# Optimization experiments

Measured on AMD Instinct MI355X. Metric: run time of the kernel, lower is better.

## Reference

```python
import jax, jax.numpy as jnp
import numpy as np

EPS = 1e-10

def _pairwise_cos_dist(X, Y):
    # X: (N, c), Y: (M, c) -> (N, M) cosine distance, matching torch impl exactly
    x_norm = jnp.sqrt(jnp.sum(X * X, axis=1, keepdims=True))          # (N, 1)
    y_norm = jnp.sqrt(jnp.sum(Y * Y, axis=1, keepdims=True)).T        # (1, M)
    return 1.0 - (X @ Y.T) / (x_norm + EPS) / (y_norm + EPS)

def _style_loss_cos(X, Y):
    D = _pairwise_cos_dist(X, Y)
    m1 = jnp.min(D, axis=1).mean()  # relaxed EMD, row mins
    m2 = jnp.min(D, axis=0).mean()  # col mins
    return jnp.maximum(m1, m2)

def _moment_loss(X, Y):
    # X, Y: (N, c)
    n = X.shape[0]
    mu_x = X.mean(axis=0, keepdims=True)
    mu_y = Y.mean(axis=0, keepdims=True)
    mu_d = jnp.abs(mu_x - mu_y).mean()
    Xc = X - mu_x
    Yc = Y - mu_y
    X_cov = (Xc.T @ Xc) / (n - 1)   # (c, c)
    Y_cov = (Yc.T @ Yc) / (n - 1)
    return mu_d + jnp.abs(X_cov - Y_cov).mean()

def _level_loss(X, Y):
    # X, Y: (N, c) per-batch, per-level feature sets
    return _style_loss_cos(X, Y) + _moment_loss(X, Y)

_per_batch_level_loss = jax.vmap(_level_loss)  # over leading batch dim

def _gather_points(feat, idx):
    # feat: (B, c, h, w), idx: (B, N) spatial indices -> (B, N, c)
    B, c, h, w = feat.shape
    flat = feat.reshape(B, c, h * w)
    g = jnp.take_along_axis(flat, idx[:, None, :], axis=2)  # (B, c, N)
    return jnp.swapaxes(g, 1, 2)

def _all_points(feat):
    # feat: (B, c, h, w) -> (B, h*w, c); used when h <= 32 (no subsampling)
    B, c, h, w = feat.shape
    return jnp.swapaxes(feat.reshape(B, c, h * w), 1, 2)

def setup_inputs() -> dict:
    key = jax.random.key(0)
    ks = jax.random.split(key, 11)
    shapes = [(8, 64, 256, 256), (8, 128, 128, 128), (8, 256, 64, 64), (8, 512, 32, 32)]
    inp = {}
    for i, s in enumerate(shapes):
        inp[f"target_feat{i}"] = jax.random.normal(ks[i], s, dtype=jnp.float32)
        inp[f"gen_feat{i}"] = jax.random.normal(ks[4 + i], s, dtype=jnp.float32)
    for j, hw in enumerate([256 * 256, 128 * 128, 64 * 64]):
        inp[f"idx{j}"] = jnp.sort(
            jax.random.randint(ks[8 + j], (8, 1000), 0, hw, dtype=jnp.int32), axis=1
        )
    return inp

def reference(target_feat0, target_feat1, target_feat2, target_feat3,
              gen_feat0, gen_feat1, gen_feat2, gen_feat3,
              idx0, idx1, idx2):
    B = target_feat0.shape[0]
    loss_b = jnp.zeros((B,), dtype=target_feat0.dtype)
    # levels 0-2: h > 32 -> subsample 1000 spatial points
    for t, g, idx in [(target_feat0, gen_feat0, idx0),
                      (target_feat1, gen_feat1, idx1),
                      (target_feat2, gen_feat2, idx2)]:
        loss_b = loss_b + _per_batch_level_loss(_gather_points(t, idx), _gather_points(g, idx))
    # level 3: h == 32 -> use all 1024 points
    loss_b = loss_b + _per_batch_level_loss(_all_points(target_feat3), _all_points(gen_feat3))
    return loss_b.mean()  # sum over batch / batch_size
```

## Files before the change

### kernel.cpp

```cpp
#include <hip/hip_runtime.h>
#include <cstdint>
#include <cstddef>

#define EPSC 1e-10f
typedef unsigned short u16;
typedef unsigned int u32;
typedef __attribute__((ext_vector_type(8))) short bf16x8;
typedef __attribute__((ext_vector_type(4))) float f32x4;

#define XTX_B 0u
#define XTY_B 7864320u
#define XNX_B 15728640u
#define XNY_B 23592960u
#define FB 15728640u
#define RNX_OFF (FB + 0u)
#define RNY_OFF (FB + 32768u)
#define RMIN_OFF (FB + 65536u)
#define CMIN_OFF (FB + 98304u)
#define MUX_OFF (FB + 131072u)
#define MUY_OFF (FB + 138752u)
#define COVS_OFF (FB + 146432u)
#define ACC_OFF (FB + 146464u)

struct Tabs { int c[4], N[4], mo[4]; u32 off[4]; };
struct GArgs {
  const float* t[4];
  const float* g[4];
  const int* idx[4];
  int c[4], hw[4], N[4];
  u32 off[4];
};

__device__ __forceinline__ u16 f2bf(float f) {
  u32 u = __float_as_uint(f);
  u = (u + 0x7fffu + ((u >> 16) & 1u)) >> 16;
  return (u16)u;
}
__device__ __forceinline__ float bf2f(u16 h) { return __uint_as_float(((u32)h) << 16); }

__global__ void k_init(float* __restrict__ wsf) {
  int i = blockIdx.x * blockDim.x + threadIdx.x;
  if (i < 65536) ((unsigned*)(wsf + RMIN_OFF))[i] = 0x7f800000u;
  if (i < 33) wsf[COVS_OFF + i] = 0.f;
}

__global__ void k_gather_all(GArgs ga, u16* __restrict__ bfb) {
  __shared__ float Ls[64 * 67];
  int y = blockIdx.y;
  int L = (y >= 7) ? 3 : (y >= 3) ? 2 : (y >= 1) ? 1 : 0;
  int ybase = (L == 0) ? 0 : (L == 1) ? 1 : (L == 2) ? 3 : 7;
  int cb64 = y - ybase;
  int c = ga.c[L], hw = ga.hw[L], N = ga.N[L];
  const int* idx = ga.idx[L];
  int z = blockIdx.z, which = z >> 3, b = z & 7;
  int c0 = cb64 * 64, n0 = blockIdx.x * 64;
  int tid = threadIdx.x;
  const float* src = which ? ga.g[L] : ga.t[L];
  u16* dt = bfb + (which ? XTY_B : XTX_B) + ga.off[L] + (size_t)b * c * 1024;
  u16* dn = bfb + (which ? XNY_B : XNX_B) + ga.off[L] + (size_t)b * c * 1024;
  int nl = tid & 63, cb = tid >> 6;
  int n = n0 + nl;
  bool nv = n < N;
  int sp = nv ? (idx ? idx[b * N + n] : n) : 0;
  const float* sbase = src + ((size_t)b * c + c0) * hw;
#pragma unroll
  for (int r = 0; r < 16; ++r) {
    int ch = cb + r * 4;
    Ls[ch * 67 + nl] = nv ? sbase[(size_t)ch * hw + sp] : 0.f;
  }
  __syncthreads();
#pragma unroll
  for (int r = 0; r < 16; ++r) {
    int ch = cb + r * 4;
    dt[(size_t)(c0 + ch) * 1024 + n] = f2bf(Ls[ch * 67 + nl]);
  }
#pragma unroll
  for (int r = 0; r < 16; ++r) {
    int nw = cb + r * 4;
    int chw = nl;
    dn[(size_t)(n0 + nw) * c + c0 + chw] = f2bf(Ls[chw * 67 + nw]);
  }
}

__global__ void k_rnorm(const u16* __restrict__ bfb, float* __restrict__ wsf, Tabs t) {
  int L = blockIdx.z;
  int c = t.c[L];
  int zy = blockIdx.y, which = zy >> 3, b = zy & 7;
  int n = blockIdx.x * 256 + threadIdx.x;
  const u16* P = bfb + (which ? XTY_B : XTX_B) + t.off[L] + (size_t)b * c * 1024;
  float s = 0.f;
  for (int ch = 0; ch < c; ch += 4) {
#pragma unroll
    for (int u = 0; u < 4; ++u) {
      float v = bf2f(P[(size_t)(ch + u) * 1024 + n]);
      s = fmaf(v, v, s);
    }
  }
  int z = L * 8 + b;
  wsf[(which ? RNY_OFF : RNX_OFF) + (size_t)z * 1024 + n] = 1.0f / (sqrtf(s) + EPSC);
}

__global__ void k_mu(const u16* __restrict__ bfb, float* __restrict__ wsf, Tabs t) {
  int L = blockIdx.z;
  int c = t.c[L], N = t.N[L];
  int zy = blockIdx.y, which = zy >> 3, b = zy & 7;
  int wv = threadIdx.x >> 6, lane = threadIdx.x & 63;
  int ch = blockIdx.x * 4 + wv;
  if (ch >= c) return;
  const u16* P = bfb + (which ? XTY_B : XTX_B) + t.off[L] + ((size_t)b * c + ch) * 1024;
  float s = 0.f;
  for (int n = lane; n < 1024; n += 64) s += bf2f(P[n]);
#pragma unroll
  for (int off = 32; off; off >>= 1) s += __shfl_down(s, off, 64);
  if (lane == 0) wsf[(which ? MUY_OFF : MUX_OFF) + t.mo[L] + (size_t)b * c + ch] = s * (1.0f / N);
}

__global__ __launch_bounds__(256) void k_cosmin(const u16* __restrict__ bfb, float* __restrict__ wsf, Tabs t) {
  __shared__ __align__(16) u16 As[128 * 72];
  __shared__ __align__(16) u16 Bs[128 * 72];
  int z = blockIdx.z, L = z >> 3, b = z & 7;
  int c = t.c[L], N = t.N[L];
  const u16* X = bfb + XNX_B + t.off[L] + (size_t)b * c * 1024;
  const u16* Y = bfb + XNY_B + t.off[L] + (size_t)b * c * 1024;
  int i0 = blockIdx.x * 128, j0 = blockIdx.y * 128;
  int tid = threadIdx.x, lane = tid & 63, w = tid >> 6;
  int wi = w >> 1, wj = w & 1, q = lane >> 4, cl = lane & 15;
  f32x4 acc[4][4] = {};
  int srow = tid >> 3, sch = tid & 7;
  for (int k0 = 0; k0 < c; k0 += 64) {
#pragma unroll
    for (int rep = 0; rep < 4; ++rep) {
      int row = srow + rep * 32;
      uint4 va = *(const uint4*)(X + (size_t)(i0 + row) * c + k0 + sch * 8);
      uint4 vb = *(const uint4*)(Y + (size_t)(j0 + row) * c + k0 + sch * 8);
      *(uint4*)(As + row * 72 + sch * 8) = va;
      *(uint4*)(Bs + row * 72 + sch * 8) = vb;
    }
    __syncthreads();
#pragma unroll
    for (int h = 0; h < 2; ++h) {
      bf16x8 af[4], bq[4];
#pragma unroll
      for (int ti = 0; ti < 4; ++ti)
        af[ti] = *(const bf16x8*)(As + (wi * 64 + ti * 16 + cl) * 72 + h * 32 + q * 8);
#pragma unroll
      for (int tj = 0; tj < 4; ++tj)
        bq[tj] = *(const bf16x8*)(Bs + (wj * 64 + tj * 16 + cl) * 72 + h * 32 + q * 8);
#pragma unroll
      for (int ti = 0; ti < 4; ++ti)
#pragma unroll
        for (int tj = 0; tj < 4; ++tj)
          acc[ti][tj] = __builtin_amdgcn_mfma_f32_16x16x32_bf16(af[ti], bq[tj], acc[ti][tj], 0, 0, 0);
    }
    __syncthreads();
  }
  const float* rnx = wsf + RNX_OFF + (size_t)z * 1024;
  const float* rny = wsf + RNY_OFF + (size_t)z * 1024;
  unsigned* rminp = (unsigned*)(wsf + RMIN_OFF) + (size_t)z * 1024;
  unsigned* cminp = (unsigned*)(wsf + CMIN_OFF) + (size_t)z * 1024;
  const float INFV = __uint_as_float(0x7f800000u);
  int colg[4]; float rnyv[4]; float colmin[4];
#pragma unroll
  for (int tj = 0; tj < 4; ++tj) {
    colg[tj] = j0 + wj * 64 + tj * 16 + cl;
    rnyv[tj] = rny[colg[tj]];
    colmin[tj] = INFV;
  }
#pragma unroll
  for (int ti = 0; ti < 4; ++ti) {
#pragma unroll
    for (int r = 0; r < 4; ++r) {
      int rowg = i0 + wi * 64 + ti * 16 + q * 4 + r;
      float rx = rnx[rowg];
      bool rv = rowg < N;
      float rmin = INFV;
#pragma unroll
      for (int tj = 0; tj < 4; ++tj) {
        float d = 1.0f - acc[ti][tj][r] * rx * rnyv[tj];
        if (!rv || colg[tj] >= N) d = INFV;
        rmin = fminf(rmin, d);
        colmin[tj] = fminf(colmin[tj], d);
      }
      rmin = fminf(rmin, __shfl_xor(rmin, 1, 64));
      rmin = fminf(rmin, __shfl_xor(rmin, 2, 64));
      rmin = fminf(rmin, __shfl_xor(rmin, 4, 64));
      rmin = fminf(rmin, __shfl_xor(rmin, 8, 64));
      if (cl == 0 && rv) atomicMin(&rminp[rowg], __float_as_uint(rmin));
    }
  }
#pragma unroll
  for (int tj = 0; tj < 4; ++tj) {
    float cm = colmin[tj];
    cm = fminf(cm, __shfl_xor(cm, 16, 64));
    cm = fminf(cm, __shfl_xor(cm, 32, 64));
    if (q == 0 && colg[tj] < N) atomicMin(&cminp[colg[tj]], __float_as_uint(cm));
  }
}

#define COVW_NBLK 370
__global__ __launch_bounds__(256) void k_covw(const u16* __restrict__ bfb, float* __restrict__ wsf, Tabs t) {
  int bid = blockIdx.x;
  int qx = COVW_NBLK >> 3, rx = COVW_NBLK & 7;
  int xcd = bid & 7, pos = bid >> 3;
  int bsw = (xcd < rx ? xcd * (qx + 1) : rx * (qx + 1) + (xcd - rx) * qx) + pos;
  int w = bsw * 4 + (threadIdx.x >> 6);
  int L, b, tt, W;
  if (w < 1088)      { int r = w;        L = 3; b = r / 136; tt = r - b * 136; W = 16; }
  else if (w < 1376) { int r = w - 1088; L = 2; b = r / 36;  tt = r - b * 36;  W = 8; }
  else if (w < 1456) { int r = w - 1376; L = 1; b = r / 10;  tt = r - b * 10;  W = 4; }
  else               { int r = w - 1456; L = 0; b = r / 3;   tt = r - b * 3;   W = 2; }
  int ti = 0, rem = tt;
  while (rem >= W - ti) { rem -= (W - ti); ++ti; }
  int tj = ti + rem;
  int c = t.c[L], N = t.N[L];
  const u16* Xp = bfb + XTX_B + t.off[L] + (size_t)b * c * 1024;
  const u16* Yp = bfb + XTY_B + t.off[L] + (size_t)b * c * 1024;
  int lane = threadIdx.x & 63, cl = lane & 15, qq = lane >> 4;
  int i0 = ti * 32, j0 = tj * 32;
  size_t aoff[2], boff[2];
#pragma unroll
  for (int u = 0; u < 2; ++u) {
    aoff[u] = (size_t)(i0 + u * 16 + cl) * 1024 + qq * 8;
    boff[u] = (size_t)(j0 + u * 16 + cl) * 1024 + qq * 8;
  }
  f32x4 acc[2][2] = {};
#pragma unroll 2
  for (int k0 = 0; k0 < 1024; k0 += 32) {
    bf16x8 ax[2], bx[2], ay[2], by[2];
#pragma unroll
    for (int u = 0; u < 2; ++u) {
      ax[u] = *(const bf16x8*)(Xp + aoff[u] + k0);
      bx[u] = *(const bf16x8*)(Xp + boff[u] + k0);
      ay[u] = *(const bf16x8*)(Yp + aoff[u] + k0);
      by[u] = *(const bf16x8*)(Yp + boff[u] + k0);
    }
#pragma unroll
    for (int u = 0; u < 2; ++u) {
      uint4 t4 = *(uint4*)&ay[u];
      t4.x ^= 0x80008000u; t4.y ^= 0x80008000u; t4.z ^= 0x80008000u; t4.w ^= 0x80008000u;
      ay[u] = *(bf16x8*)&t4;
    }
#pragma unroll
    for (int u = 0; u < 2; ++u)
#pragma unroll
      for (int v = 0; v < 2; ++v) {
        acc[u][v] = __builtin_amdgcn_mfma_f32_16x16x32_bf16(ax[u], bx[v], acc[u][v], 0, 0, 0);
        acc[u][v] = __builtin_amdgcn_mfma_f32_16x16x32_bf16(ay[u], by[v], acc[u][v], 0, 0, 0);
      }
  }
  const float* mux = wsf + MUX_OFF + t.mo[L] + (size_t)b * c;
  const float* muy = wsf + MUY_OFF + t.mo[L] + (size_t)b * c;
  float fN = (float)N, inv1 = 1.0f / (float)(N - 1);
  float mxj[2], myj[2];
#pragma unroll
  for (int v = 0; v < 2; ++v) {
    int jg = j0 + v * 16 + cl;
    mxj[v] = mux[jg]; myj[v] = muy[jg];
  }
  float s = 0.f;
#pragma unroll
  for (int u = 0; u < 2; ++u)
#pragma unroll
    for (int r = 0; r < 4; ++r) {
      int ig = i0 + u * 16 + qq * 4 + r;
      float mxi = mux[ig], myi = muy[ig];
#pragma unroll
      for (int v = 0; v < 2; ++v) {
        float d = (acc[u][v][r] - fN * (mxi * mxj[v] - myi * myj[v])) * inv1;
        s += fabsf(d);
      }
    }
  if (ti != tj) s += s;
#pragma unroll
  for (int o = 1; o < 64; o <<= 1) s += __shfl_xor(s, o, 64);
  if (lane == 0) atomicAdd(&wsf[COVS_OFF + (L * 8 + b)], s);
}

__global__ void k_final(float* __restrict__ wsf, Tabs t) {
  __shared__ float red[4];
  int z = blockIdx.x, L = z >> 3, b = z & 7;
  int c = t.c[L], N = t.N[L];
  const unsigned* rmin = (const unsigned*)(wsf + RMIN_OFF) + (size_t)z * 1024;
  const unsigned* cmin = (const unsigned*)(wsf + CMIN_OFF) + (size_t)z * 1024;
  const float* mux = wsf + MUX_OFF + t.mo[L] + (size_t)b * c;
  const float* muy = wsf + MUY_OFF + t.mo[L] + (size_t)b * c;
  int tid = threadIdx.x;
  float sr = 0.f, sc = 0.f, sm = 0.f;
  for (int n = tid; n < N; n += 256) {
    sr += __uint_as_float(rmin[n]);
    sc += __uint_as_float(cmin[n]);
  }
  for (int ch = tid; ch < c; ch += 256) sm += fabsf(mux[ch] - muy[ch]);
  float vals[3] = {sr, sc, sm};
  float tot[3] = {0.f, 0.f, 0.f};
  for (int qq = 0; qq < 3; ++qq) {
    float v = vals[qq];
#pragma unroll
    for (int off = 32; off; off >>= 1) v += __shfl_down(v, off, 64);
    if ((tid & 63) == 0) red[tid >> 6] = v;
    __syncthreads();
    if (tid == 0) tot[qq] = red[0] + red[1] + red[2] + red[3];
    __syncthreads();
  }
  if (tid == 0) {
    float style = fmaxf(tot[0] / (float)N, tot[1] / (float)N);
    float mu_d = tot[2] / (float)c;
    float cov = wsf[COVS_OFF + z] / ((float)c * (float)c);
    atomicAdd(&wsf[ACC_OFF], style + mu_d + cov);
  }
}

__global__ void k_out(const float* __restrict__ wsf, float* __restrict__ out) {
  if (threadIdx.x == 0 && blockIdx.x == 0) out[0] = wsf[ACC_OFF] * 0.125f;
}

extern "C" void kernel_launch(void* const* d_in, const int* in_sizes, int n_in,
                              void* d_out, int out_size, void* d_ws, size_t ws_size,
                              hipStream_t stream) {
  (void)in_sizes; (void)n_in; (void)out_size; (void)ws_size;
  static const int LC[4] = {64, 128, 256, 512};
  static const int LN[4] = {1000, 1000, 1000, 1024};
  static const int LHW[4] = {65536, 16384, 4096, 1024};
  static const u32 LOFF[4] = {0u, 524288u, 1572864u, 3670016u};
  static const int MO[4] = {0, 512, 1536, 3584};

  float* wsf = (float*)d_ws;
  u16* bfb = (u16*)d_ws;
  Tabs t;
  GArgs ga;
  for (int L = 0; L < 4; ++L) {
    t.c[L] = LC[L]; t.N[L] = LN[L]; t.mo[L] = MO[L]; t.off[L] = LOFF[L];
    ga.t[L] = (const float*)d_in[2 * L];
    ga.g[L] = (const float*)d_in[2 * L + 1];
    ga.idx[L] = (L < 3) ? (const int*)d_in[8 + L] : nullptr;
    ga.c[L] = LC[L]; ga.hw[L] = LHW[L]; ga.N[L] = LN[L]; ga.off[L] = LOFF[L];
  }

  k_init<<<dim3(256), dim3(256), 0, stream>>>(wsf);
  k_gather_all<<<dim3(16, 15, 16), dim3(256), 0, stream>>>(ga, bfb);
  k_rnorm<<<dim3(4, 16, 4), dim3(256), 0, stream>>>(bfb, wsf, t);
  k_mu<<<dim3(128, 16, 4), dim3(256), 0, stream>>>(bfb, wsf, t);
  k_cosmin<<<dim3(8, 8, 32), dim3(256), 0, stream>>>(bfb, wsf, t);
  k_covw<<<dim3(COVW_NBLK), dim3(256), 0, stream>>>(bfb, wsf, t);
  k_final<<<dim3(32), dim3(256), 0, stream>>>(wsf, t);
  k_out<<<dim3(1), dim3(64), 0, stream>>>(wsf, (float*)d_out);
}
```

Measured before the change: 598.5 us.

## Fuse norm and mean reductions into gather; load cosine-min MFMA operands directly

Sums of squares per point and per-channel sums are now accumulated with atomics inside the gather kernel from the fp32 values. This removes the separate k_rnorm and k_mu passes, which re-read the bf16 buffers. The reciprocal norm is now computed at use in k_cosmin, and the mean scaling is folded into the covariance and final kernels. k_cosmin also drops its LDS staging and barriers and feeds MFMAs straight from global memory. The costs are extra atomic traffic in the gather and possibly worse operand reuse and latency hiding in the GEMM.

```diff
diff --git a/kernel.cpp b/kernel.cpp
--- a/kernel.cpp
+++ b/kernel.cpp
@@ -27,7 +27,7 @@
   const float* t[4];
   const float* g[4];
   const int* idx[4];
-  int c[4], hw[4], N[4];
+  int c[4], hw[4], N[4], mo[4];
   u32 off[4];
 };
 
@@ -41,11 +41,13 @@
 __global__ void k_init(float* __restrict__ wsf) {
   int i = blockIdx.x * blockDim.x + threadIdx.x;
   if (i < 65536) ((unsigned*)(wsf + RMIN_OFF))[i] = 0x7f800000u;
-  if (i < 33) wsf[COVS_OFF + i] = 0.f;
-}
-
-__global__ void k_gather_all(GArgs ga, u16* __restrict__ bfb) {
+  if (i < 65536) wsf[RNX_OFF + i] = 0.f;
+  if (i < 15393) wsf[MUX_OFF + i] = 0.f;
+}
+
+__global__ void k_gather_all(GArgs ga, u16* __restrict__ bfb, float* __restrict__ wsf) {
   __shared__ float Ls[64 * 67];
+  __shared__ float Rs[64];
   int y = blockIdx.y;
   int L = (y >= 7) ? 3 : (y >= 3) ? 2 : (y >= 1) ? 1 : 0;
   int ybase = (L == 0) ? 0 : (L == 1) ? 1 : (L == 2) ? 3 : 7;
@@ -58,17 +60,33 @@
   const float* src = which ? ga.g[L] : ga.t[L];
   u16* dt = bfb + (which ? XTY_B : XTX_B) + ga.off[L] + (size_t)b * c * 1024;
   u16* dn = bfb + (which ? XNY_B : XNX_B) + ga.off[L] + (size_t)b * c * 1024;
+  float* musum = wsf + (which ? MUY_OFF : MUX_OFF) + ga.mo[L] + (size_t)b * c + c0;
+  float* rnsum = wsf + (which ? RNY_OFF : RNX_OFF) + (size_t)(L * 8 + b) * 1024 + n0;
   int nl = tid & 63, cb = tid >> 6;
   int n = n0 + nl;
   bool nv = n < N;
   int sp = nv ? (idx ? idx[b * N + n] : n) : 0;
   const float* sbase = src + ((size_t)b * c + c0) * hw;
+  float v[16];
 #pragma unroll
   for (int r = 0; r < 16; ++r) {
     int ch = cb + r * 4;
-    Ls[ch * 67 + nl] = nv ? sbase[(size_t)ch * hw + sp] : 0.f;
+    v[r] = nv ? sbase[(size_t)ch * hw + sp] : 0.f;
+    Ls[ch * 67 + nl] = v[r];
+  }
+  if (tid < 64) Rs[tid] = 0.f;
+  float s2 = 0.f;
+#pragma unroll
+  for (int r = 0; r < 16; ++r) s2 = fmaf(v[r], v[r], s2);
+#pragma unroll
+  for (int r = 0; r < 16; ++r) {
+    float s = v[r];
+#pragma unroll
+    for (int off = 32; off; off >>= 1) s += __shfl_down(s, off, 64);
+    if (nl == 0) atomicAdd(&musum[cb + r * 4], s);
   }
   __syncthreads();
+  atomicAdd(&Rs[nl], s2);
 #pragma unroll
   for (int r = 0; r < 16; ++r) {
     int ch = cb + r * 4;
@@ -80,44 +98,11 @@
     int chw = nl;
     dn[(size_t)(n0 + nw) * c + c0 + chw] = f2bf(Ls[chw * 67 + nw]);
   }
-}
-
-__global__ void k_rnorm(const u16* __restrict__ bfb, float* __restrict__ wsf, Tabs t) {
-  int L = blockIdx.z;
-  int c = t.c[L];
-  int zy = blockIdx.y, which = zy >> 3, b = zy & 7;
-  int n = blockIdx.x * 256 + threadIdx.x;
-  const u16* P = bfb + (which ? XTY_B : XTX_B) + t.off[L] + (size_t)b * c * 1024;
-  float s = 0.f;
-  for (int ch = 0; ch < c; ch += 4) {
-#pragma unroll
-    for (int u = 0; u < 4; ++u) {
-      float v = bf2f(P[(size_t)(ch + u) * 1024 + n]);
-      s = fmaf(v, v, s);
-    }
-  }
-  int z = L * 8 + b;
-  wsf[(which ? RNY_OFF : RNX_OFF) + (size_t)z * 1024 + n] = 1.0f / (sqrtf(s) + EPSC);
-}
-
-__global__ void k_mu(const u16* __restrict__ bfb, float* __restrict__ wsf, Tabs t) {
-  int L = blockIdx.z;
-  int c = t.c[L], N = t.N[L];
-  int zy = blockIdx.y, which = zy >> 3, b = zy & 7;
-  int wv = threadIdx.x >> 6, lane = threadIdx.x & 63;
-  int ch = blockIdx.x * 4 + wv;
-  if (ch >= c) return;
-  const u16* P = bfb + (which ? XTY_B : XTX_B) + t.off[L] + ((size_t)b * c + ch) * 1024;
-  float s = 0.f;
-  for (int n = lane; n < 1024; n += 64) s += bf2f(P[n]);
-#pragma unroll
-  for (int off = 32; off; off >>= 1) s += __shfl_down(s, off, 64);
-  if (lane == 0) wsf[(which ? MUY_OFF : MUX_OFF) + t.mo[L] + (size_t)b * c + ch] = s * (1.0f / N);
+  __syncthreads();
+  if (tid < 64) atomicAdd(&rnsum[tid], Rs[tid]);
 }
 
 __global__ __launch_bounds__(256) void k_cosmin(const u16* __restrict__ bfb, float* __restrict__ wsf, Tabs t) {
-  __shared__ __align__(16) u16 As[128 * 72];
-  __shared__ __align__(16) u16 Bs[128 * 72];
   int z = blockIdx.z, L = z >> 3, b = z & 7;
   int c = t.c[L], N = t.N[L];
   const u16* X = bfb + XNX_B + t.off[L] + (size_t)b * c * 1024;
@@ -125,34 +110,25 @@
   int i0 = blockIdx.x * 128, j0 = blockIdx.y * 128;
   int tid = threadIdx.x, lane = tid & 63, w = tid >> 6;
   int wi = w >> 1, wj = w & 1, q = lane >> 4, cl = lane & 15;
+  const u16* ap[4];
+  const u16* bp[4];
+#pragma unroll
+  for (int u = 0; u < 4; ++u) {
+    ap[u] = X + (size_t)(i0 + wi * 64 + u * 16 + cl) * c + q * 8;
+    bp[u] = Y + (size_t)(j0 + wj * 64 + u * 16 + cl) * c + q * 8;
+  }
   f32x4 acc[4][4] = {};
-  int srow = tid >> 3, sch = tid & 7;
-  for (int k0 = 0; k0 < c; k0 += 64) {
-#pragma unroll
-    for (int rep = 0; rep < 4; ++rep) {
-      int row = srow + rep * 32;
-      uint4 va = *(const uint4*)(X + (size_t)(i0 + row) * c + k0 + sch * 8);
-      uint4 vb = *(const uint4*)(Y + (size_t)(j0 + row) * c + k0 + sch * 8);
-      *(uint4*)(As + row * 72 + sch * 8) = va;
-      *(uint4*)(Bs + row * 72 + sch * 8) = vb;
-    }
-    __syncthreads();
-#pragma unroll
-    for (int h = 0; h < 2; ++h) {
-      bf16x8 af[4], bq[4];
-#pragma unroll
-      for (int ti = 0; ti < 4; ++ti)
-        af[ti] = *(const bf16x8*)(As + (wi * 64 + ti * 16 + cl) * 72 + h * 32 + q * 8);
+  for (int k0 = 0; k0 < c; k0 += 32) {
+    bf16x8 af[4], bq4[4];
+#pragma unroll
+    for (int u = 0; u < 4; ++u) af[u] = *(const bf16x8*)(ap[u] + k0);
+#pragma unroll
+    for (int u = 0; u < 4; ++u) bq4[u] = *(const bf16x8*)(bp[u] + k0);
+#pragma unroll
+    for (int ti = 0; ti < 4; ++ti)
 #pragma unroll
       for (int tj = 0; tj < 4; ++tj)
-        bq[tj] = *(const bf16x8*)(Bs + (wj * 64 + tj * 16 + cl) * 72 + h * 32 + q * 8);
-#pragma unroll
-      for (int ti = 0; ti < 4; ++ti)
-#pragma unroll
-        for (int tj = 0; tj < 4; ++tj)
-          acc[ti][tj] = __builtin_amdgcn_mfma_f32_16x16x32_bf16(af[ti], bq[tj], acc[ti][tj], 0, 0, 0);
-    }
-    __syncthreads();
+        acc[ti][tj] = __builtin_amdgcn_mfma_f32_16x16x32_bf16(af[ti], bq4[tj], acc[ti][tj], 0, 0, 0);
   }
   const float* rnx = wsf + RNX_OFF + (size_t)z * 1024;
   const float* rny = wsf + RNY_OFF + (size_t)z * 1024;
@@ -163,7 +139,7 @@
 #pragma unroll
   for (int tj = 0; tj < 4; ++tj) {
     colg[tj] = j0 + wj * 64 + tj * 16 + cl;
-    rnyv[tj] = rny[colg[tj]];
+    rnyv[tj] = 1.0f / (sqrtf(rny[colg[tj]]) + EPSC);
     colmin[tj] = INFV;
   }
 #pragma unroll
@@ -171,7 +147,7 @@
 #pragma unroll
     for (int r = 0; r < 4; ++r) {
       int rowg = i0 + wi * 64 + ti * 16 + q * 4 + r;
-      float rx = rnx[rowg];
+      float rx = 1.0f / (sqrtf(rnx[rowg]) + EPSC);
       bool rv = rowg < N;
       float rmin = INFV;
 #pragma unroll
@@ -250,7 +226,7 @@
   }
   const float* mux = wsf + MUX_OFF + t.mo[L] + (size_t)b * c;
   const float* muy = wsf + MUY_OFF + t.mo[L] + (size_t)b * c;
-  float fN = (float)N, inv1 = 1.0f / (float)(N - 1);
+  float fN = (float)N, inv1 = 1.0f / (float)(N - 1), invN = 1.0f / fN;
   float mxj[2], myj[2];
 #pragma unroll
   for (int v = 0; v < 2; ++v) {
@@ -266,7 +242,7 @@
       float mxi = mux[ig], myi = muy[ig];
 #pragma unroll
       for (int v = 0; v < 2; ++v) {
-        float d = (acc[u][v][r] - fN * (mxi * mxj[v] - myi * myj[v])) * inv1;
+        float d = (acc[u][v][r] - (mxi * mxj[v] - myi * myj[v]) * invN) * inv1;
         s += fabsf(d);
       }
     }
@@ -304,7 +280,7 @@
   }
   if (tid == 0) {
     float style = fmaxf(tot[0] / (float)N, tot[1] / (float)N);
-    float mu_d = tot[2] / (float)c;
+    float mu_d = tot[2] / ((float)N * (float)c);
     float cov = wsf[COVS_OFF + z] / ((float)c * (float)c);
     atomicAdd(&wsf[ACC_OFF], style + mu_d + cov);
   }
@@ -333,13 +309,11 @@
     ga.t[L] = (const float*)d_in[2 * L];
     ga.g[L] = (const float*)d_in[2 * L + 1];
     ga.idx[L] = (L < 3) ? (const int*)d_in[8 + L] : nullptr;
-    ga.c[L] = LC[L]; ga.hw[L] = LHW[L]; ga.N[L] = LN[L]; ga.off[L] = LOFF[L];
+    ga.c[L] = LC[L]; ga.hw[L] = LHW[L]; ga.N[L] = LN[L]; ga.mo[L] = MO[L]; ga.off[L] = LOFF[L];
   }
 
   k_init<<<dim3(256), dim3(256), 0, stream>>>(wsf);
-  k_gather_all<<<dim3(16, 15, 16), dim3(256), 0, stream>>>(ga, bfb);
-  k_rnorm<<<dim3(4, 16, 4), dim3(256), 0, stream>>>(bfb, wsf, t);
-  k_mu<<<dim3(128, 16, 4), dim3(256), 0, stream>>>(bfb, wsf, t);
+  k_gather_all<<<dim3(16, 15, 16), dim3(256), 0, stream>>>(ga, bfb, wsf);
   k_cosmin<<<dim3(8, 8, 32), dim3(256), 0, stream>>>(bfb, wsf, t);
   k_covw<<<dim3(COVW_NBLK), dim3(256), 0, stream>>>(bfb, wsf, t);
   k_final<<<dim3(32), dim3(256), 0, stream>>>(wsf, t);
```

Measured after the change: 575.4 us. 3.9% less time.
